# Kernel tuning notes

Hardware: AMD Instinct MI355X
Metric: run time of the kernel (lower is better)

## Reference

```python
import jax, jax.numpy as jnp
import numpy as np

M, K, N = 8192, 4096, 4096
DIV = 1.0 / (127.0 * 127.0)


def setup_inputs() -> dict:
    key = jax.random.key(0)
    k1, k2, k3, k4, k5 = jax.random.split(key, 5)
    x = jax.random.randint(k1, (M, K), -127, 128, dtype=jnp.int8)
    weight_int8 = jax.random.randint(k2, (N, K), -127, 128, dtype=jnp.int8)
    scale_x = jnp.abs(jax.random.normal(k3, (M,), dtype=jnp.float32)) * 0.01
    scale_w = jnp.abs(jax.random.normal(k4, (N,), dtype=jnp.float32)) * 0.01
    bias = (jax.random.normal(k5, (N,), dtype=jnp.float32) * 0.01).astype(jnp.float16)
    return {"x": x, "scale_x": scale_x, "weight_int8": weight_int8,
            "scale_w": scale_w, "bias": bias}


def reference(x, scale_x, weight_int8, scale_w, bias):
    # int8 GEMM with int32 accumulation: [M,K] @ [K,N]
    acc = jax.lax.dot_general(
        x, weight_int8.T,
        dimension_numbers=(((1,), (0,)), ((), ())),
        preferred_element_type=jnp.int32,
    ).astype(jnp.float32)
    # fused rowwise/colwise dequant + bias, cast to fp16
    out = acc * DIV * scale_x[:, None] * scale_w[None, :] + bias.astype(jnp.float32)[None, :]
    return out.astype(jnp.float16)
```

## Files before the change

### kernel.cpp

```cpp
#include <hip/hip_runtime.h>
#include <hip/hip_fp16.h>
#include <cstdint>
#include <cstddef>

#define M_DIM 8192
#define N_DIM 4096
#define K_DIM 4096

typedef int v4i __attribute__((ext_vector_type(4)));

__global__ __launch_bounds__(256) void pack_i32_to_i8(const int* __restrict__ srcX,
                                                      uint32_t* __restrict__ dstX,
                                                      const int* __restrict__ srcW,
                                                      uint32_t* __restrict__ dstW,
                                                      int nx4, int ntot) {
    int i = blockIdx.x * 256 + threadIdx.x;
    if (i >= ntot) return;
    const int* s;
    uint32_t*  d;
    int j;
    if (i < nx4) { s = srcX; d = dstX; j = i; }
    else         { s = srcW; d = dstW; j = i - nx4; }
    int4 a = ((const int4*)s)[j];
#if __has_builtin(__builtin_amdgcn_perm)
    uint32_t lo = __builtin_amdgcn_perm((uint32_t)a.y, (uint32_t)a.x, 0x0400);
    uint32_t hi = __builtin_amdgcn_perm((uint32_t)a.w, (uint32_t)a.z, 0x0400);
    d[j] = __builtin_amdgcn_perm(hi, lo, 0x05040100);
#else
    d[j] = (uint32_t)(a.x & 0xff) | ((uint32_t)(a.y & 0xff) << 8) |
           ((uint32_t)(a.z & 0xff) << 16) | ((uint32_t)a.w << 24);
#endif
}

__device__ __forceinline__ void gload_lds16(const int8_t* g, int8_t* l) {
    __builtin_amdgcn_global_load_lds(
        (const __attribute__((address_space(1))) void*)g,
        (__attribute__((address_space(3))) void*)l, 16, 0, 0);
}


#define VMW(n) asm volatile("s_waitcnt vmcnt(" #n ")" ::: "memory")

#define PH_MFMA(MBASE)                                                        \
    __builtin_amdgcn_s_setprio(1);                                            \
    _Pragma("unroll")                                                         \
    for (int mi = 0; mi < 4; ++mi) {                                          \
        _Pragma("unroll")                                                     \
        for (int ni = 0; ni < 4; ++ni)                                        \
            acc[(MBASE) + mi][ni] = __builtin_amdgcn_mfma_i32_16x16x64_i8(    \
                af[mi], bf[ni], acc[(MBASE) + mi][ni], 0, 0, 0);              \
    }                                                                         \
    __builtin_amdgcn_s_setprio(0);

#define KTILE(KT, DO_STAGE, VMSTMT)                                           \
    do {                                                                      \
        int8_t* bufA = lds + ((KT) & 3) * 32768;                              \
        int8_t* bufB = bufA + 16384;                                          \
        v4i af[4], bf[4];                                                     \
                  \
        _Pragma("unroll")                                                     \
        for (int i = 0; i < 4; ++i) {                                         \
            af[i] = *(const v4i*)(bufA + aoff + i * 1024);                    \
            bf[i] = *(const v4i*)(bufB + boff + i * 1024);                    \
        }                                                                     \
        if (DO_STAGE) {                                                       \
            int8_t* sAb = lds + (((KT) + 3) & 3) * 32768;                     \
            gload_lds16(gA0 + ((KT) + 3) * 64, sAb + ldsoff);                 \
            gload_lds16(gA1 + ((KT) + 3) * 64, sAb + ldsoff + 8192);          \
        }                                                                     \
        __builtin_amdgcn_s_barrier();                                         \
        asm volatile("s_waitcnt lgkmcnt(0)" ::: "memory");                    \
        __builtin_amdgcn_sched_barrier(0);                                    \
        PH_MFMA(0)                                                            \
        __builtin_amdgcn_s_barrier();                                         \
                  \
        _Pragma("unroll")                                                     \
        for (int i = 0; i < 4; ++i)                                           \
            af[i] = *(const v4i*)(bufA + aoff + 4096 + i * 1024);             \
        if (DO_STAGE) {                                                       \
            int8_t* sBb = lds + (((KT) + 3) & 3) * 32768 + 16384;             \
            gload_lds16(gB0 + ((KT) + 3) * 64, sBb + ldsoff);                 \
            gload_lds16(gB1 + ((KT) + 3) * 64, sBb + ldsoff + 8192);          \
        }                                                                     \
        __builtin_amdgcn_s_barrier();                                         \
        asm volatile("s_waitcnt lgkmcnt(0)" ::: "memory");                    \
        __builtin_amdgcn_sched_barrier(0);                                    \
        PH_MFMA(4)                                                            \
        VMSTMT;                                                               \
        __builtin_amdgcn_s_barrier();                                         \
    } while (0)

__global__ __launch_bounds__(512, 2) void gemm_i8_dq(const int8_t* __restrict__ A,
                                                     const int8_t* __restrict__ W,
                                                     const float* __restrict__ sx,
                                                     const float* __restrict__ sw,
                                                     const float* __restrict__ bias,
                                                     float* __restrict__ out) {
    __shared__ __attribute__((aligned(16))) int8_t lds[131072];

    const int t    = threadIdx.x;
    const int lane = t & 63;
    const int w    = t >> 6;
    const int wm   = w >> 2;
    const int wn   = w & 3;

    const int flat = blockIdx.y * 16 + blockIdx.x;
    const int xcd  = flat & 7;
    const int idx  = flat >> 3;
    const int bm   = (xcd >> 1) * 8 + (idx & 7);
    const int bn   = (xcd & 1) * 8 + (idx >> 3);

    const int srow   = t >> 2;
    const int rot    = (srow >> 1) & 3;
    const int gchunk = ((t & 3) + rot) & 3;
    const int scol   = gchunk * 16;
    const int8_t* gA0 = A + (size_t)(bm * 256 + srow) * K_DIM + scol;
    const int8_t* gA1 = gA0 + (size_t)128 * K_DIM;
    const int8_t* gB0 = W + (size_t)(bn * 256 + srow) * K_DIM + scol;
    const int8_t* gB1 = gB0 + (size_t)128 * K_DIM;
    const int ldsoff = t * 16;

    const int rho  = lane & 15;
    const int p16  = (((lane >> 4) - (rho >> 1)) & 3) * 16;
    const int aoff = (wm * 128 + rho) * 64 + p16;
    const int boff = (wn * 64 + rho) * 64 + p16;

    v4i acc[8][4];
    const v4i vzero = {0, 0, 0, 0};
#pragma unroll
    for (int mi = 0; mi < 8; mi++)
#pragma unroll
        for (int ni = 0; ni < 4; ni++) acc[mi][ni] = vzero;

#pragma unroll
    for (int pt = 0; pt < 3; ++pt) {
        int8_t* bufA = lds + pt * 32768;
        int8_t* bufB = bufA + 16384;
        gload_lds16(gA0 + pt * 64, bufA + ldsoff);
        gload_lds16(gA1 + pt * 64, bufA + ldsoff + 8192);
        gload_lds16(gB0 + pt * 64, bufB + ldsoff);
        gload_lds16(gB1 + pt * 64, bufB + ldsoff + 8192);
    }
    VMW(8);
    __builtin_amdgcn_s_barrier();

    for (int kt = 0; kt < 61; ++kt) KTILE(kt, true, VMW(8));
    KTILE(61, false, VMW(4));
    KTILE(62, false, VMW(0));
    KTILE(63, false, ((void)0));

    const float DIVF = (float)(1.0 / (127.0 * 127.0));
    const int col0 = bn * 256 + wn * 64 + (lane & 15);
    const int row0 = bm * 256 + wm * 128 + (lane >> 4) * 4;

    float swv[4], bv[4];
#pragma unroll
    for (int ni = 0; ni < 4; ni++) {
        swv[ni] = sw[col0 + ni * 16];
        bv[ni]  = bias[col0 + ni * 16];
    }

#pragma unroll
    for (int mi = 0; mi < 8; mi++) {
#pragma unroll
        for (int r = 0; r < 4; r++) {
            const int row = row0 + mi * 16 + r;
            const float xs = sx[row];
#pragma unroll
            for (int ni = 0; ni < 4; ni++) {
                float v = __fmul_rn((float)acc[mi][ni][r], DIVF);
                v = __fmul_rn(v, xs);
                v = __fmul_rn(v, swv[ni]);
                v = __fadd_rn(v, bv[ni]);
                out[(size_t)row * N_DIM + col0 + ni * 16] = __half2float(__float2half(v));
            }
        }
    }
}

extern "C" void kernel_launch(void* const* d_in, const int* in_sizes, int n_in,
                              void* d_out, int out_size, void* d_ws, size_t ws_size,
                              hipStream_t stream) {
    const int*   x_i32 = (const int*)d_in[0];
    const float* sx    = (const float*)d_in[1];
    const int*   w_i32 = (const int*)d_in[2];
    const float* sw    = (const float*)d_in[3];
    const float* bias  = (const float*)d_in[4];
    float* out = (float*)d_out;

    uint8_t* xb = (uint8_t*)d_ws;
    uint8_t* wb = (uint8_t*)d_ws + (size_t)M_DIM * K_DIM;

    const int nx4  = (M_DIM * K_DIM) / 4;
    const int nw4  = (N_DIM * K_DIM) / 4;
    const int ntot = nx4 + nw4;
    pack_i32_to_i8<<<(ntot + 255) / 256, 256, 0, stream>>>(
        x_i32, (uint32_t*)xb, w_i32, (uint32_t*)wb, nx4, ntot);

    dim3 grid(N_DIM / 256, M_DIM / 256);
    gemm_i8_dq<<<grid, 512, 0, stream>>>((const int8_t*)xb, (const int8_t*)wb,
                                         sx, sw, bias, out);
}
```

Before: 392.9 us.

## Collapse per-k-tile sync to one barrier and issue all LDS reads upfront

Each k-tile previously ran as two phases, each with its own barriers, explicit lgkmcnt waits and a separate A-fragment reload. The k-tile now loads all A and B fragments (including the second A half into extra registers) at the start, issues all four global-to-LDS stage loads together, runs all 32 MFMAs, and finishes with a single vmcnt wait and one barrier. Dropping the last barrier is safe because four LDS buffers are used with a prefetch distance of three. The change is meant to cut barrier and wait overhead and let the compiler overlap LDS reads with MFMAs, at the cost of higher VGPR pressure under launch_bounds(512,2).

```diff
diff --git a/kernel.cpp b/kernel.cpp
--- a/kernel.cpp
+++ b/kernel.cpp
@@ -41,53 +41,48 @@
 
 #define VMW(n) asm volatile("s_waitcnt vmcnt(" #n ")" ::: "memory")
 
-#define PH_MFMA(MBASE)                                                        \
-    __builtin_amdgcn_s_setprio(1);                                            \
-    _Pragma("unroll")                                                         \
-    for (int mi = 0; mi < 4; ++mi) {                                          \
-        _Pragma("unroll")                                                     \
-        for (int ni = 0; ni < 4; ++ni)                                        \
-            acc[(MBASE) + mi][ni] = __builtin_amdgcn_mfma_i32_16x16x64_i8(    \
-                af[mi], bf[ni], acc[(MBASE) + mi][ni], 0, 0, 0);              \
-    }                                                                         \
-    __builtin_amdgcn_s_setprio(0);
-
-#define KTILE(KT, DO_STAGE, VMSTMT)                                           \
+#define KTILE(KT, DO_STAGE, VMSTMT, DO_SYNC)                                  \
     do {                                                                      \
-        int8_t* bufA = lds + ((KT) & 3) * 32768;                              \
-        int8_t* bufB = bufA + 16384;                                          \
-        v4i af[4], bf[4];                                                     \
-                  \
+        const int8_t* bufA = lds + ((KT) & 3) * 32768;                        \
+        const int8_t* bufB = bufA + 16384;                                    \
+        v4i af[4], bf[4], a2[4];                                              \
         _Pragma("unroll")                                                     \
         for (int i = 0; i < 4; ++i) {                                         \
             af[i] = *(const v4i*)(bufA + aoff + i * 1024);                    \
             bf[i] = *(const v4i*)(bufB + boff + i * 1024);                    \
         }                                                                     \
+        _Pragma("unroll")                                                     \
+        for (int i = 0; i < 4; ++i)                                           \
+            a2[i] = *(const v4i*)(bufA + aoff + 4096 + i * 1024);             \
         if (DO_STAGE) {                                                       \
             int8_t* sAb = lds + (((KT) + 3) & 3) * 32768;                     \
             gload_lds16(gA0 + ((KT) + 3) * 64, sAb + ldsoff);                 \
             gload_lds16(gA1 + ((KT) + 3) * 64, sAb + ldsoff + 8192);          \
+            gload_lds16(gB0 + ((KT) + 3) * 64, sAb + 16384 + ldsoff);         \
+            gload_lds16(gB1 + ((KT) + 3) * 64, sAb + 16384 + ldsoff + 8192);  \
         }                                                                     \
-        __builtin_amdgcn_s_barrier();                                         \
-        asm volatile("s_waitcnt lgkmcnt(0)" ::: "memory");                    \
-        __builtin_amdgcn_sched_barrier(0);                                    \
-        PH_MFMA(0)                                                            \
-        __builtin_amdgcn_s_barrier();                                         \
-                  \
+        __builtin_amdgcn_s_setprio(1);                                        \
         _Pragma("unroll")                                                     \
-        for (int i = 0; i < 4; ++i)                                           \
-            af[i] = *(const v4i*)(bufA + aoff + 4096 + i * 1024);             \
-        if (DO_STAGE) {                                                       \
-            int8_t* sBb = lds + (((KT) + 3) & 3) * 32768 + 16384;             \
-            gload_lds16(gB0 + ((KT) + 3) * 64, sBb + ldsoff);                 \
-            gload_lds16(gB1 + ((KT) + 3) * 64, sBb + ldsoff + 8192);          \
+        for (int mi = 0; mi < 4; ++mi) {                                      \
+            _Pragma("unroll")                                                 \
+            for (int ni = 0; ni < 4; ++ni)                                    \
+                acc[mi][ni] = __builtin_amdgcn_mfma_i32_16x16x64_i8(          \
+                    af[mi], bf[ni], acc[mi][ni], 0, 0, 0);                    \
         }                                                                     \
-        __builtin_amdgcn_s_barrier();                                         \
-        asm volatile("s_waitcnt lgkmcnt(0)" ::: "memory");                    \
-        __builtin_amdgcn_sched_barrier(0);                                    \
-        PH_MFMA(4)                                                            \
-        VMSTMT;                                                               \
-        __builtin_amdgcn_s_barrier();                                         \
+        _Pragma("unroll")                                                     \
+        for (int mi = 0; mi < 4; ++mi) {                                      \
+            _Pragma("unroll")                                                 \
+            for (int ni = 0; ni < 4; ++ni)                                    \
+                acc[4 + mi][ni] = __builtin_amdgcn_mfma_i32_16x16x64_i8(      \
+                    a2[mi], bf[ni], acc[4 + mi][ni], 0, 0, 0);                \
+        }                                                                     \
+        __builtin_amdgcn_s_setprio(0);                                        \
+        if (DO_SYNC) {                                                        \
+            __builtin_amdgcn_sched_barrier(0);                                \
+            VMSTMT;                                                           \
+            __builtin_amdgcn_s_barrier();                                     \
+            __builtin_amdgcn_sched_barrier(0);                                \
+        }                                                                     \
     } while (0)
 
 __global__ __launch_bounds__(512, 2) void gemm_i8_dq(const int8_t* __restrict__ A,
@@ -143,11 +138,12 @@
     }
     VMW(8);
     __builtin_amdgcn_s_barrier();
+    __builtin_amdgcn_sched_barrier(0);
 
-    for (int kt = 0; kt < 61; ++kt) KTILE(kt, true, VMW(8));
-    KTILE(61, false, VMW(4));
-    KTILE(62, false, VMW(0));
-    KTILE(63, false, ((void)0));
+    for (int kt = 0; kt < 61; ++kt) KTILE(kt, true, VMW(8), true);
+    KTILE(61, false, VMW(4), true);
+    KTILE(62, false, VMW(0), true);
+    KTILE(63, false, ((void)0), false);
 
     const float DIVF = (float)(1.0 / (127.0 * 127.0));
     const int col0 = bn * 256 + wn * 64 + (lane & 15);
```

Result: no change. 386.6 us (-1.6%).
